# Optimization experiments

Measured on AMD Instinct MI355X. Metric: run time of the kernel, lower is better.

The kernel has to match this reference:

```python
import jax, jax.numpy as jnp
import numpy as np

K = 64  # num_struct_elements


def rational_hat(pts, mask, centers, radius):
    """pts: (B,P,D), mask: (B,P), centers: (K,D), radius: scalar -> (B,K).

    f(x,c) = 1/(1+||x-c||_1) - 1/(1+| |r| - ||x-c||_1 |), masked sum over points.
    """
    # L1 distance to every center: (B,P,K)
    d = jnp.sum(jnp.abs(pts[:, :, None, :] - centers[None, None, :, :]), axis=-1)
    f = 1.0 / (1.0 + d) - 1.0 / (1.0 + jnp.abs(jnp.abs(radius) - d))
    # mask dummy points and reduce over the point axis -> (B,K)
    return jnp.einsum('bpk,bp->bk', f, mask)


def setup_inputs() -> dict:
    key = jax.random.key(0)
    ks = jax.random.split(key, 6)
    B, P0, PE = 128, 4096, 1024
    inp = {
        'h_0': jax.random.normal(ks[0], (B, P0, 2), dtype=jnp.float32),
        'mask_0': jnp.ones((B, P0), dtype=jnp.float32),
        'h_0_ess': jax.random.normal(ks[1], (B, PE, 1), dtype=jnp.float32),
        'mask_0_ess': jnp.ones((B, PE), dtype=jnp.float32),
        'h_1_ess': jax.random.normal(ks[2], (B, PE, 1), dtype=jnp.float32),
        'mask_1_ess': jnp.ones((B, PE), dtype=jnp.float32),
        # learned parameters: centers ~ N(0,1) (torchph default init), radius init 0.1
        'centers_0': jax.random.normal(ks[3], (K, 2), dtype=jnp.float32),
        'radius_0': jnp.float32(0.1),
        'centers_0_ess': jax.random.normal(ks[4], (K, 1), dtype=jnp.float32),
        'radius_0_ess': jnp.float32(0.1),
        'centers_1_ess': jax.random.normal(ks[5], (K, 1), dtype=jnp.float32),
        'radius_1_ess': jnp.float32(0.1),
    }
    return inp


def reference(h_0, mask_0, h_0_ess, mask_0_ess, h_1_ess, mask_1_ess,
              centers_0, radius_0, centers_0_ess, radius_0_ess,
              centers_1_ess, radius_1_ess):
    x0 = rational_hat(h_0, mask_0, centers_0, radius_0)
    x0e = rational_hat(h_0_ess, mask_0_ess, centers_0_ess, radius_0_ess)
    x1e = rational_hat(h_1_ess, mask_1_ess, centers_1_ess, radius_1_ess)
    return jnp.concatenate([x0, x0e, x1e], axis=1)  # (B, 3K)
```

## Files before the change

kernel.cpp:

```cpp
#include <hip/hip_runtime.h>

#define TPB 256
#define NW  (TPB / 64)
#define PPB 1024
#define PPW (PPB / NW)

__global__ __launch_bounds__(TPB) void pershom_kernel(
    const float* __restrict__ h0,  const float* __restrict__ m0,
    const float* __restrict__ h0e, const float* __restrict__ m0e,
    const float* __restrict__ h1e, const float* __restrict__ m1e,
    const float* __restrict__ c0,  const float* __restrict__ r0,
    const float* __restrict__ c0e, const float* __restrict__ r0e,
    const float* __restrict__ c1e, const float* __restrict__ r1e,
    float* __restrict__ out)
{
    __shared__ float4 pts[PPB];
    __shared__ float  partial[NW][64];

    const int bid = blockIdx.x;
    const int tid = threadIdx.x;
    const int k   = tid & 63;
    const int sub = tid >> 6;

    const float* h; const float* m; const float* cen; const float* rad;
    int outidx, D;
    if (bid < 512) {
        int b = bid >> 2, p0 = (bid & 3) * PPB;
        h = h0 + (size_t)(b * 4096 + p0) * 2; m = m0 + b * 4096 + p0;
        cen = c0; rad = r0; outidx = b * 192 + k; D = 2;
    } else if (bid < 640) {
        int b = bid - 512;
        h = h0e + b * 1024; m = m0e + b * 1024;
        cen = c0e; rad = r0e; outidx = b * 192 + 64 + k; D = 1;
    } else {
        int b = bid - 640;
        h = h1e + b * 1024; m = m1e + b * 1024;
        cen = c1e; rad = r1e; outidx = b * 192 + 128 + k; D = 1;
    }

    if (D == 2) {
        const float2* src = (const float2*)h;
        for (int i = tid; i < PPB; i += TPB) {
            float2 xy = src[i];
            pts[i] = make_float4(xy.x, xy.y, m[i], 0.f);
        }
    } else {
        for (int i = tid; i < PPB; i += TPB) {
            pts[i] = make_float4(h[i], 0.f, m[i], 0.f);
        }
    }

    float cx, cy;
    if (D == 2) { cx = cen[2 * k]; cy = cen[2 * k + 1]; }
    else        { cx = cen[k];     cy = 0.f; }
    const float R = fabsf(rad[0]);

    __syncthreads();

    float acc0 = 0.f, acc1 = 0.f;
    const int base = sub * PPW;
    if (D == 2) {
        #pragma unroll 8
        for (int i = 0; i < PPW; ++i) {
            float4 pt = pts[base + i];
            float d   = fabsf(pt.x - cx) + fabsf(pt.y - cy);
            float t   = R - d;
            float num = fabsf(t) - d;
            float den = (1.f + d) * (1.f + fabsf(t));
            float c   = (pt.z * num) * __builtin_amdgcn_rcpf(den);
            if (i & 1) acc1 += c; else acc0 += c;
        }
    } else {
        #pragma unroll 8
        for (int i = 0; i < PPW; ++i) {
            float4 pt = pts[base + i];
            float d   = fabsf(pt.x - cx);
            float t   = R - d;
            float num = fabsf(t) - d;
            float den = (1.f + d) * (1.f + fabsf(t));
            float c   = (pt.z * num) * __builtin_amdgcn_rcpf(den);
            if (i & 1) acc1 += c; else acc0 += c;
        }
    }

    partial[sub][k] = acc0 + acc1;
    __syncthreads();
    if (tid < 64) {
        float s = partial[0][tid] + partial[1][tid]
                + partial[2][tid] + partial[3][tid];
        atomicAdd(&out[outidx], s);
    }
}

extern "C" void kernel_launch(void* const* d_in, const int* in_sizes, int n_in,
                              void* d_out, int out_size, void* d_ws, size_t ws_size,
                              hipStream_t stream) {
    const float* h0  = (const float*)d_in[0];
    const float* m0  = (const float*)d_in[1];
    const float* h0e = (const float*)d_in[2];
    const float* m0e = (const float*)d_in[3];
    const float* h1e = (const float*)d_in[4];
    const float* m1e = (const float*)d_in[5];
    const float* c0  = (const float*)d_in[6];
    const float* r0  = (const float*)d_in[7];
    const float* c0e = (const float*)d_in[8];
    const float* r0e = (const float*)d_in[9];
    const float* c1e = (const float*)d_in[10];
    const float* r1e = (const float*)d_in[11];
    float* out = (float*)d_out;

    dim3 grid(512 + 128 + 128);
    dim3 block(TPB);
    pershom_kernel<<<grid, block, 0, stream>>>(
        h0, m0, h0e, m0e, h1e, m1e, c0, r0, c0e, r0e, c1e, r1e, out);
}
```

Before: 96.83 us.

## Pack points densely in LDS and read mask via uniform global vector loads

```diff
diff --git a/kernel.cpp b/kernel.cpp
--- a/kernel.cpp
+++ b/kernel.cpp
@@ -1,9 +1,8 @@
 #include <hip/hip_runtime.h>
 
 #define TPB 256
-#define NW  (TPB / 64)
+#define NW  4
 #define PPB 1024
-#define PPW (PPB / NW)
 
 __global__ __launch_bounds__(TPB) void pershom_kernel(
     const float* __restrict__ h0,  const float* __restrict__ m0,
@@ -14,7 +13,7 @@
     const float* __restrict__ c1e, const float* __restrict__ r1e,
     float* __restrict__ out)
 {
-    __shared__ float4 pts[PPB];
+    __shared__ float4 pts[512];
     __shared__ float  partial[NW][64];
 
     const int bid = blockIdx.x;
@@ -38,17 +37,9 @@
         cen = c1e; rad = r1e; outidx = b * 192 + 128 + k; D = 1;
     }
 
-    if (D == 2) {
-        const float2* src = (const float2*)h;
-        for (int i = tid; i < PPB; i += TPB) {
-            float2 xy = src[i];
-            pts[i] = make_float4(xy.x, xy.y, m[i], 0.f);
-        }
-    } else {
-        for (int i = tid; i < PPB; i += TPB) {
-            pts[i] = make_float4(h[i], 0.f, m[i], 0.f);
-        }
-    }
+    const float4* src = (const float4*)h;
+    const int nvec = (D == 2) ? 512 : 256;
+    for (int i = tid; i < nvec; i += TPB) pts[i] = src[i];
 
     float cx, cy;
     if (D == 2) { cx = cen[2 * k]; cy = cen[2 * k + 1]; }
@@ -57,29 +48,54 @@
 
     __syncthreads();
 
+    const int subu = __builtin_amdgcn_readfirstlane(sub);
+
     float acc0 = 0.f, acc1 = 0.f;
-    const int base = sub * PPW;
     if (D == 2) {
-        #pragma unroll 8
-        for (int i = 0; i < PPW; ++i) {
-            float4 pt = pts[base + i];
-            float d   = fabsf(pt.x - cx) + fabsf(pt.y - cy);
-            float t   = R - d;
-            float num = fabsf(t) - d;
-            float den = (1.f + d) * (1.f + fabsf(t));
-            float c   = (pt.z * num) * __builtin_amdgcn_rcpf(den);
-            if (i & 1) acc1 += c; else acc0 += c;
+        const float2* msk = (const float2*)m;
+        const int base = subu * 128;
+        #pragma unroll 4
+        for (int j = 0; j < 128; ++j) {
+            float4 q  = pts[base + j];
+            float2 mm = msk[base + j];
+            float d0 = fabsf(q.x - cx) + fabsf(q.y - cy);
+            float t0 = R - d0;
+            float n0 = fabsf(t0) - d0;
+            float e0 = (1.f + d0) * (1.f + fabsf(t0));
+            acc0 += (mm.x * n0) * __builtin_amdgcn_rcpf(e0);
+            float d1 = fabsf(q.z - cx) + fabsf(q.w - cy);
+            float t1 = R - d1;
+            float n1 = fabsf(t1) - d1;
+            float e1 = (1.f + d1) * (1.f + fabsf(t1));
+            acc1 += (mm.y * n1) * __builtin_amdgcn_rcpf(e1);
         }
     } else {
-        #pragma unroll 8
-        for (int i = 0; i < PPW; ++i) {
-            float4 pt = pts[base + i];
-            float d   = fabsf(pt.x - cx);
-            float t   = R - d;
-            float num = fabsf(t) - d;
-            float den = (1.f + d) * (1.f + fabsf(t));
-            float c   = (pt.z * num) * __builtin_amdgcn_rcpf(den);
-            if (i & 1) acc1 += c; else acc0 += c;
+        const float4* msk = (const float4*)m;
+        const int base = subu * 64;
+        #pragma unroll 4
+        for (int j = 0; j < 64; ++j) {
+            float4 q  = pts[base + j];
+            float4 mm = msk[base + j];
+            float d0 = fabsf(q.x - cx);
+            float t0 = R - d0;
+            float n0 = fabsf(t0) - d0;
+            float e0 = (1.f + d0) * (1.f + fabsf(t0));
+            acc0 += (mm.x * n0) * __builtin_amdgcn_rcpf(e0);
+            float d1 = fabsf(q.y - cx);
+            float t1 = R - d1;
+            float n1 = fabsf(t1) - d1;
+            float e1 = (1.f + d1) * (1.f + fabsf(t1));
+            acc1 += (mm.y * n1) * __builtin_amdgcn_rcpf(e1);
+            float d2 = fabsf(q.z - cx);
+            float t2 = R - d2;
+            float n2 = fabsf(t2) - d2;
+            float e2 = (1.f + d2) * (1.f + fabsf(t2));
+            acc0 += (mm.z * n2) * __builtin_amdgcn_rcpf(e2);
+            float d3 = fabsf(q.w - cx);
+            float t3 = R - d3;
+            float n3 = fabsf(t3) - d3;
+            float e3 = (1.f + d3) * (1.f + fabsf(t3));
+            acc1 += (mm.w * n3) * __builtin_amdgcn_rcpf(e3);
         }
     }
 
```

Measured after the change: 95.37 us. No clear change (-1.5%).
